# Optimization experiments

Hardware: AMD Instinct MI355X
Metric: run time of the kernel (lower is better)

Reference implementation:

```python
import jax, jax.numpy as jnp
import numpy as np


def setup_inputs() -> dict:
    key = jax.random.key(0)
    k1, k2, k3, k4 = jax.random.split(key, 4)
    B, S, H, P = 8, 2048, 1024, 4096
    hidden_states = jax.random.normal(k1, (B, S, H), dtype=jnp.float32)
    pairs = jax.random.randint(k2, (B, P, 2), 0, S, dtype=jnp.int64)
    # classifier params: Linear(2H -> H), Linear(H -> 2). Stored as (in, out).
    W1 = jax.random.normal(k3, (2 * H, H), dtype=jnp.float32) * (1.0 / np.sqrt(2 * H))
    b1 = jnp.zeros((H,), dtype=jnp.float32)
    W2 = jax.random.normal(k4, (H, 2), dtype=jnp.float32) * (1.0 / np.sqrt(H))
    b2 = jnp.zeros((2,), dtype=jnp.float32)
    return {"hidden_states": hidden_states, "pairs": pairs,
            "W1": W1, "b1": b1, "W2": W2, "b2": b2}


def reference(hidden_states, pairs, W1, b1, W2, b2):
    # Gather pair embeddings: (B, P, H) each.
    emb1 = jnp.take_along_axis(hidden_states, pairs[:, :, 0:1], axis=1)
    emb2 = jnp.take_along_axis(hidden_states, pairs[:, :, 1:2], axis=1)
    pair_emb = jnp.concatenate([emb1, emb2], axis=-1)  # (B, P, 2H)
    h = jnp.einsum('bpi,ih->bph', pair_emb, W1) + b1
    h = jax.nn.gelu(h, approximate=False)  # torch nn.GELU default is exact erf
    # Dropout is identity at inference.
    logits = jnp.einsum('bph,ho->bpo', h, W2) + b2  # (B, P, 2)
    return logits
```

## Files before the change

### kernel.cpp

```cpp
#include <hip/hip_runtime.h>
#include <hip/hip_bf16.h>

#define B_  8
#define S_  2048
#define H_  1024
#define P_  4096
#define K_  2048
#define M_  32768

typedef unsigned short u16;
using bf16x8 = __attribute__((ext_vector_type(8))) short;
using f32x4  = __attribute__((ext_vector_type(4))) float;

#define AS1 __attribute__((address_space(1)))
#define AS3 __attribute__((address_space(3)))

__device__ inline u16 f2bf(float f) {
  union { float f; unsigned u; } c; c.f = f;
  unsigned u = c.u;
  unsigned r = (u + 0x7fffu + ((u >> 16) & 1u)) >> 16;
  return (u16)r;
}

__global__ void cvt_hidden_k(const float4* __restrict__ src,
                             ushort4* __restrict__ dst, int n4) {
  int i = blockIdx.x * blockDim.x + threadIdx.x;
  int stride = gridDim.x * blockDim.x;
  for (; i < n4; i += stride) {
    float4 v = src[i];
    ushort4 o;
    o.x = f2bf(v.x); o.y = f2bf(v.y); o.z = f2bf(v.z); o.w = f2bf(v.w);
    dst[i] = o;
  }
}

__global__ void transp_w1_k(const float* __restrict__ w1, u16* __restrict__ w1t) {
  __shared__ float tile[32][33];
  int n0 = blockIdx.x * 32;
  int k0 = blockIdx.y * 32;
  int tx = threadIdx.x;
  int ty = threadIdx.y;
#pragma unroll
  for (int i = 0; i < 32; i += 8)
    tile[ty + i][tx] = w1[(size_t)(k0 + ty + i) * H_ + n0 + tx];
  __syncthreads();
#pragma unroll
  for (int i = 0; i < 32; i += 8)
    w1t[(size_t)(n0 + ty + i) * K_ + k0 + tx] = f2bf(tile[tx][ty + i]);
}

__global__ __launch_bounds__(512, 2) void gemm_k(
    const u16*  __restrict__ hidB,
    const u16*  __restrict__ w1t,
    const int*  __restrict__ pairs,
    const float* __restrict__ b1,
    const float2* __restrict__ w2,
    float*      __restrict__ part)
{
  __shared__ u16 lds[65536];

#define REG(SLOT, KS, AB) ((((SLOT)*2 + (KS))*2 + (AB)) * 8192)

  int orig = blockIdx.x;
  int bid = (orig & 7) * 64 + (orig >> 3);
  int nt = bid & 3;
  int mt = bid >> 2;
  int n0 = nt * 256;
  int m0 = mt * 256;
  int bI = m0 >> 12;
  int pp = m0 & 4095;

  int t = threadIdx.x;
  int w = t >> 6;
  int l = t & 63;
  int lr = l & 15;
  int lj = l >> 4;
  int wr = w >> 2;
  int wn = w & 3;

  int slot8 = (lj ^ ((l >> 1) & 3)) * 8;
  int gsrc = (l & 3) ^ ((l >> 3) & 3);

  int r0 = w * 16 + (l >> 2);
  int r1 = 128 + r0;

  int2 sv0 = ((const int2*)pairs)[bI * P_ + pp + r0];
  int2 sv1 = ((const int2*)pairs)[bI * P_ + pp + r1];

  const u16* hidBase = hidB + ((size_t)bI << 21);

  f32x4 acc[8][4];
#pragma unroll
  for (int i = 0; i < 8; ++i)
#pragma unroll
    for (int j = 0; j < 4; ++j)
      acc[i][j] = (f32x4){0.f, 0.f, 0.f, 0.f};

  auto STAGE_A = [&](int base, int tile, int ks) {
    int k = tile * 64 + ks * 32;
    int kcol = k & 1023;
    int half = k >> 10;
    int sA0 = half ? sv0.y : sv0.x;
    int sA1 = half ? sv1.y : sv1.x;
    int dst = base + w * 512 + l * 8;
    __builtin_amdgcn_global_load_lds(
        (const AS1 void*)(hidBase + (((size_t)sA0) << 10) + kcol + gsrc * 8),
        (AS3 void*)&lds[dst], 16, 0, 0);
    __builtin_amdgcn_global_load_lds(
        (const AS1 void*)(hidBase + (((size_t)sA1) << 10) + kcol + gsrc * 8),
        (AS3 void*)&lds[dst + 4096], 16, 0, 0);
  };
  auto STAGE_B = [&](int base, int tile, int ks) {
    int k = tile * 64 + ks * 32;
    int dst = base + w * 512 + l * 8;
    __builtin_amdgcn_global_load_lds(
        (const AS1 void*)(w1t + (size_t)(n0 + r0) * K_ + k + gsrc * 8),
        (AS3 void*)&lds[dst], 16, 0, 0);
    __builtin_amdgcn_global_load_lds(
        (const AS1 void*)(w1t + (size_t)(n0 + r1) * K_ + k + gsrc * 8),
        (AS3 void*)&lds[dst + 4096], 16, 0, 0);
  };

#define VM6 asm volatile("s_waitcnt vmcnt(6)" ::: "memory")
#define VM4 asm volatile("s_waitcnt vmcnt(4)" ::: "memory")
#define VM0 asm volatile("s_waitcnt vmcnt(0)" ::: "memory")

  bf16x8 bv[4];

#define PHASE(SLOT, KS, MH, STAGEOP, WAITOP)                                   \
  {                                                                            \
    bf16x8 af[4];                                                              \
    _Pragma("unroll")                                                          \
    for (int mi = 0; mi < 4; ++mi)                                             \
      af[mi] = *(const bf16x8*)&lds[REG(SLOT, KS, 0) +                         \
          (wr * 128 + (MH) * 64 + mi * 16 + lr) * 32 + slot8];                 \
    if ((MH) == 0) {                                                           \
      _Pragma("unroll")                                                        \
      for (int ni = 0; ni < 4; ++ni)                                           \
        bv[ni] = *(const bf16x8*)&lds[REG(SLOT, KS, 1) +                       \
            (wn * 64 + ni * 16 + lr) * 32 + slot8];                            \
    }                                                                          \
    STAGEOP;                                                                   \
    WAITOP;                                                                    \
    __builtin_amdgcn_s_barrier();                                              \
    asm volatile("s_waitcnt lgkmcnt(0)" ::: "memory");                         \
    __builtin_amdgcn_sched_barrier(0);                                         \
    __builtin_amdgcn_s_setprio(1);                                             \
    _Pragma("unroll")                                                          \
    for (int mi = 0; mi < 4; ++mi)                                             \
      _Pragma("unroll")                                                        \
      for (int ni = 0; ni < 4; ++ni)                                           \
        acc[(MH) * 4 + mi][ni] = __builtin_amdgcn_mfma_f32_16x16x32_bf16(      \
            af[mi], bv[ni], acc[(MH) * 4 + mi][ni], 0, 0, 0);                  \
    __builtin_amdgcn_s_setprio(0);                                             \
    __builtin_amdgcn_s_barrier();                                              \
  }

  STAGE_A(REG(0, 0, 0), 0, 0); STAGE_B(REG(0, 0, 1), 0, 0);
  STAGE_A(REG(0, 1, 0), 0, 1); STAGE_B(REG(0, 1, 1), 0, 1);
  STAGE_A(REG(1, 0, 0), 1, 0); STAGE_B(REG(1, 0, 1), 1, 0);
  asm volatile("s_waitcnt vmcnt(8)" ::: "memory");
  __builtin_amdgcn_s_barrier();

  for (int u = 0; u < 15; ++u) {
    int t1 = 2 * u + 1, t2 = 2 * u + 2, t3 = 2 * u + 3;
    PHASE(0, 0, 0, STAGE_A(REG(1, 1, 0), t1, 1), VM6);
    PHASE(0, 0, 1, STAGE_B(REG(1, 1, 1), t1, 1), );
    PHASE(0, 1, 0, STAGE_A(REG(0, 0, 0), t2, 0), VM6);
    PHASE(0, 1, 1, STAGE_B(REG(0, 0, 1), t2, 0), );
    PHASE(1, 0, 0, STAGE_A(REG(0, 1, 0), t2, 1), VM6);
    PHASE(1, 0, 1, STAGE_B(REG(0, 1, 1), t2, 1), );
    PHASE(1, 1, 0, STAGE_A(REG(1, 0, 0), t3, 0), VM6);
    PHASE(1, 1, 1, STAGE_B(REG(1, 0, 1), t3, 0), );
  }
  PHASE(0, 0, 0, STAGE_A(REG(1, 1, 0), 31, 1), VM6);
  PHASE(0, 0, 1, STAGE_B(REG(1, 1, 1), 31, 1), );
  PHASE(0, 1, 0, , VM4);
  PHASE(0, 1, 1, , );
  PHASE(1, 0, 0, , VM0);
  PHASE(1, 0, 1, , );
  PHASE(1, 1, 0, , );
  PHASE(1, 1, 1, , );
#undef PHASE

  int q = nt * 4 + wn;
  float2* pOut = (float2*)part;
#pragma unroll
  for (int mi = 0; mi < 8; ++mi) {
    float s0[4] = {0.f, 0.f, 0.f, 0.f};
    float s1[4] = {0.f, 0.f, 0.f, 0.f};
#pragma unroll
    for (int ni = 0; ni < 4; ++ni) {
      int n = n0 + wn * 64 + ni * 16 + lr;
      float bb = b1[n];
      float2 wv = w2[n];
#pragma unroll
      for (int j = 0; j < 4; ++j) {
        float x = acc[mi][ni][j] + bb;
        float g = 0.5f * x * (1.0f + erff(x * 0.70710678118654752f));
        s0[j] += g * wv.x;
        s1[j] += g * wv.y;
      }
    }
#pragma unroll
    for (int off = 1; off < 16; off <<= 1) {
#pragma unroll
      for (int j = 0; j < 4; ++j) {
        s0[j] += __shfl_xor(s0[j], off, 64);
        s1[j] += __shfl_xor(s1[j], off, 64);
      }
    }
    if (lr == 0) {
#pragma unroll
      for (int j = 0; j < 4; ++j) {
        int m = m0 + wr * 128 + mi * 16 + lj * 4 + j;
        pOut[((size_t)q << 15) + m] = make_float2(s0[j], s1[j]);
      }
    }
  }
}

__global__ void reduce_k(const float2* __restrict__ part,
                         const float* __restrict__ b2,
                         float2* __restrict__ out) {
  int m = blockIdx.x * blockDim.x + threadIdx.x;
  if (m >= M_) return;
  float a0 = b2[0], a1 = b2[1];
#pragma unroll
  for (int q = 0; q < 16; ++q) {
    float2 v = part[((size_t)q << 15) + m];
    a0 += v.x; a1 += v.y;
  }
  out[m] = make_float2(a0, a1);
}

extern "C" void kernel_launch(void* const* d_in, const int* in_sizes, int n_in,
                              void* d_out, int out_size, void* d_ws, size_t ws_size,
                              hipStream_t stream) {
  const float* hidden = (const float*)d_in[0];
  const int*   pairs  = (const int*)d_in[1];
  const float* W1     = (const float*)d_in[2];
  const float* b1     = (const float*)d_in[3];
  const float* W2     = (const float*)d_in[4];
  const float* b2     = (const float*)d_in[5];
  float* out = (float*)d_out;

  u16* hidB = (u16*)d_ws;
  u16* w1t  = hidB + (size_t)B_ * S_ * H_;
  float* part = (float*)(w1t + (size_t)H_ * K_);

  int n4 = (B_ * S_ * H_) / 4;
  cvt_hidden_k<<<4096, 256, 0, stream>>>((const float4*)hidden, (ushort4*)hidB, n4);
  transp_w1_k<<<dim3(H_ / 32, K_ / 32), dim3(32, 8), 0, stream>>>(W1, w1t);
  gemm_k<<<(M_ / 256) * (H_ / 256), 512, 0, stream>>>(
      hidB, w1t, pairs, b1, (const float2*)W2, part);
  reduce_k<<<(M_ + 255) / 256, 256, 0, stream>>>(
      (const float2*)part, b2, (float2*)out);
}
```

Baseline: 173.3 us.

## Merge half-phases into one phase per k-slice with fewer barriers

Each k-slice was processed as two phases split by M-half, each with its own pair of barriers and one staging op. The two halves are now merged into a single phase that loads all A fragments for both halves plus B, stages both A and B loads, then issues all 32 MFMAs. The vmcnt waits are adjusted to match. This halves the barrier count and lengthens the MFMA run between syncs, at the cost of more live fragment registers and coarser overlap of loads with compute.

```diff
diff --git a/kernel.cpp b/kernel.cpp
--- a/kernel.cpp
+++ b/kernel.cpp
@@ -121,25 +121,23 @@
         (AS3 void*)&lds[dst + 4096], 16, 0, 0);
   };
 
-#define VM6 asm volatile("s_waitcnt vmcnt(6)" ::: "memory")
+#define VM8 asm volatile("s_waitcnt vmcnt(8)" ::: "memory")
 #define VM4 asm volatile("s_waitcnt vmcnt(4)" ::: "memory")
 #define VM0 asm volatile("s_waitcnt vmcnt(0)" ::: "memory")
 
-  bf16x8 bv[4];
-
-#define PHASE(SLOT, KS, MH, STAGEOP, WAITOP)                                   \
+#define PHASE(SLOT, KS, STAGEOP, WAITOP)                                       \
   {                                                                            \
-    bf16x8 af[4];                                                              \
+    bf16x8 af[2][4], bv[4];                                                    \
     _Pragma("unroll")                                                          \
-    for (int mi = 0; mi < 4; ++mi)                                             \
-      af[mi] = *(const bf16x8*)&lds[REG(SLOT, KS, 0) +                         \
-          (wr * 128 + (MH) * 64 + mi * 16 + lr) * 32 + slot8];                 \
-    if ((MH) == 0) {                                                           \
+    for (int MH = 0; MH < 2; ++MH)                                             \
       _Pragma("unroll")                                                        \
-      for (int ni = 0; ni < 4; ++ni)                                           \
-        bv[ni] = *(const bf16x8*)&lds[REG(SLOT, KS, 1) +                       \
-            (wn * 64 + ni * 16 + lr) * 32 + slot8];                            \
-    }                                                                          \
+      for (int mi = 0; mi < 4; ++mi)                                           \
+        af[MH][mi] = *(const bf16x8*)&lds[REG(SLOT, KS, 0) +                   \
+            (wr * 128 + MH * 64 + mi * 16 + lr) * 32 + slot8];                 \
+    _Pragma("unroll")                                                          \
+    for (int ni = 0; ni < 4; ++ni)                                             \
+      bv[ni] = *(const bf16x8*)&lds[REG(SLOT, KS, 1) +                         \
+          (wn * 64 + ni * 16 + lr) * 32 + slot8];                              \
     STAGEOP;                                                                   \
     WAITOP;                                                                    \
     __builtin_amdgcn_s_barrier();                                              \
@@ -147,11 +145,13 @@
     __builtin_amdgcn_sched_barrier(0);                                         \
     __builtin_amdgcn_s_setprio(1);                                             \
     _Pragma("unroll")                                                          \
-    for (int mi = 0; mi < 4; ++mi)                                             \
+    for (int MH = 0; MH < 2; ++MH)                                             \
       _Pragma("unroll")                                                        \
-      for (int ni = 0; ni < 4; ++ni)                                           \
-        acc[(MH) * 4 + mi][ni] = __builtin_amdgcn_mfma_f32_16x16x32_bf16(      \
-            af[mi], bv[ni], acc[(MH) * 4 + mi][ni], 0, 0, 0);                  \
+      for (int mi = 0; mi < 4; ++mi)                                           \
+        _Pragma("unroll")                                                      \
+        for (int ni = 0; ni < 4; ++ni)                                         \
+          acc[MH * 4 + mi][ni] = __builtin_amdgcn_mfma_f32_16x16x32_bf16(      \
+              af[MH][mi], bv[ni], acc[MH * 4 + mi][ni], 0, 0, 0);              \
     __builtin_amdgcn_s_setprio(0);                                             \
     __builtin_amdgcn_s_barrier();                                              \
   }
@@ -159,28 +159,20 @@
   STAGE_A(REG(0, 0, 0), 0, 0); STAGE_B(REG(0, 0, 1), 0, 0);
   STAGE_A(REG(0, 1, 0), 0, 1); STAGE_B(REG(0, 1, 1), 0, 1);
   STAGE_A(REG(1, 0, 0), 1, 0); STAGE_B(REG(1, 0, 1), 1, 0);
-  asm volatile("s_waitcnt vmcnt(8)" ::: "memory");
+  VM8;
   __builtin_amdgcn_s_barrier();
 
   for (int u = 0; u < 15; ++u) {
     int t1 = 2 * u + 1, t2 = 2 * u + 2, t3 = 2 * u + 3;
-    PHASE(0, 0, 0, STAGE_A(REG(1, 1, 0), t1, 1), VM6);
-    PHASE(0, 0, 1, STAGE_B(REG(1, 1, 1), t1, 1), );
-    PHASE(0, 1, 0, STAGE_A(REG(0, 0, 0), t2, 0), VM6);
-    PHASE(0, 1, 1, STAGE_B(REG(0, 0, 1), t2, 0), );
-    PHASE(1, 0, 0, STAGE_A(REG(0, 1, 0), t2, 1), VM6);
-    PHASE(1, 0, 1, STAGE_B(REG(0, 1, 1), t2, 1), );
-    PHASE(1, 1, 0, STAGE_A(REG(1, 0, 0), t3, 0), VM6);
-    PHASE(1, 1, 1, STAGE_B(REG(1, 0, 1), t3, 0), );
-  }
-  PHASE(0, 0, 0, STAGE_A(REG(1, 1, 0), 31, 1), VM6);
-  PHASE(0, 0, 1, STAGE_B(REG(1, 1, 1), 31, 1), );
-  PHASE(0, 1, 0, , VM4);
-  PHASE(0, 1, 1, , );
-  PHASE(1, 0, 0, , VM0);
-  PHASE(1, 0, 1, , );
-  PHASE(1, 1, 0, , );
-  PHASE(1, 1, 1, , );
+    PHASE(0, 0, { STAGE_A(REG(1,1,0), t1, 1); STAGE_B(REG(1,1,1), t1, 1); }, VM8);
+    PHASE(0, 1, { STAGE_A(REG(0,0,0), t2, 0); STAGE_B(REG(0,0,1), t2, 0); }, VM8);
+    PHASE(1, 0, { STAGE_A(REG(0,1,0), t2, 1); STAGE_B(REG(0,1,1), t2, 1); }, VM8);
+    PHASE(1, 1, { STAGE_A(REG(1,0,0), t3, 0); STAGE_B(REG(1,0,1), t3, 0); }, VM8);
+  }
+  PHASE(0, 0, { STAGE_A(REG(1,1,0), 31, 1); STAGE_B(REG(1,1,1), 31, 1); }, VM8);
+  PHASE(0, 1, , VM8);
+  PHASE(1, 0, , VM4);
+  PHASE(1, 1, , VM0);
 #undef PHASE
 
   int q = nt * 4 + wn;
```

New measurement: 174.4 us. No clear change (+0.6%).
